# Optimization experiments

Measured on AMD Instinct MI355X. Metric: run time of the kernel, lower is better.

## Reference

```python
import jax, jax.numpy as jnp
import numpy as np

D_MODEL = 1024
N_HEADS = 16
HEAD_DIM = D_MODEL // N_HEADS
NEG = -10000.0  # module uses -10000, not -inf


def setup_inputs() -> dict:
    key = jax.random.key(0)
    ks = jax.random.split(key, 8)
    B, T = 4, 2048
    q = jax.random.normal(ks[0], (B, T, D_MODEL), dtype=jnp.float32)
    k = jax.random.normal(ks[1], (B, T, D_MODEL), dtype=jnp.float32)
    v = jax.random.normal(ks[2], (B, T, D_MODEL), dtype=jnp.float32)
    attn_mask = jnp.ones((B, T), dtype=jnp.float32)
    # xavier_uniform for square [d, d] weights: limit = sqrt(6/(d+d))
    lim = float(np.sqrt(6.0 / (D_MODEL + D_MODEL)))
    Wq = jax.random.uniform(ks[3], (D_MODEL, D_MODEL), jnp.float32, -lim, lim)
    Wk = jax.random.uniform(ks[4], (D_MODEL, D_MODEL), jnp.float32, -lim, lim)
    Wv = jax.random.uniform(ks[5], (D_MODEL, D_MODEL), jnp.float32, -lim, lim)
    Wo = jax.random.uniform(ks[6], (D_MODEL, D_MODEL), jnp.float32, -lim, lim)
    return {"q": q, "k": k, "v": v, "attn_mask": attn_mask,
            "Wq": Wq, "Wk": Wk, "Wv": Wv, "Wo": Wo, "mask_future": 1}


def _split_heads(x):
    B, T, _ = x.shape
    return x.reshape(B, T, N_HEADS, HEAD_DIM).transpose(0, 2, 1, 3)  # [B,H,T,D]


def reference(q, k, v, attn_mask, Wq, Wk, Wv, Wo, mask_future):
    # torch Linear: y = x @ W.T  (weights stored [out, in])
    qh = _split_heads(jnp.einsum('btd,ed->bte', q, Wq))
    kh = _split_heads(jnp.einsum('btd,ed->bte', k, Wk))
    vh = _split_heads(jnp.einsum('btd,ed->bte', v, Wv))
    L, S = qh.shape[-2], kh.shape[-2]
    # dual scale: each of q and k scaled by 1/d**0.25
    scale = 1.0 / jnp.sqrt(jnp.sqrt(jnp.float32(HEAD_DIM)))
    scores = jnp.einsum('bhld,bhsd->bhls', qh * scale, kh * scale)
    if mask_future:
        causal_bias = jnp.triu(jnp.full((L, S), NEG, dtype=scores.dtype), k=1)
        scores = scores + causal_bias
    # padding mask: attn_mask [B, S] -> broadcast [B,1,1,S]; 0 entries -> -10000
    pad = attn_mask[:, None, None, :]
    scores = jnp.where(pad == 0, jnp.asarray(NEG, scores.dtype), scores)
    probs = jax.nn.softmax(scores, axis=-1)  # dropout p=0.0 -> identity
    ctx = jnp.einsum('bhls,bhsd->bhld', probs, vh)
    B = ctx.shape[0]
    ctx = ctx.transpose(0, 2, 1, 3).reshape(B, L, D_MODEL)
    return jnp.einsum('btd,ed->bte', ctx, Wo)
```

## Files before the change

### kernel.cpp

```cpp
#include <hip/hip_runtime.h>

typedef unsigned short u16;
typedef __attribute__((ext_vector_type(8))) _Float16 f16x8;
typedef __attribute__((ext_vector_type(2))) __fp16 fp16v2;
typedef __attribute__((ext_vector_type(4))) float f32x4;

#define T_SEQ 2048
#define NH 16
#define DH 64
#define DM 1024
#define NEG2 (-14426.95f)
#define QS2 (0.42466089f)

__device__ __forceinline__ unsigned pk2(float a, float b) {
  union { fp16v2 v; unsigned u; } c;
  c.v = __builtin_amdgcn_cvt_pkrtz(a, b);
  return c.u;
}
__device__ __forceinline__ u16 f2h(float a) {
  union { _Float16 h; u16 u; } c; c.h = (_Float16)a; return c.u;
}

__device__ __forceinline__ void async_load16(const void* g, void* l) {
  __builtin_amdgcn_global_load_lds(
      (const __attribute__((address_space(1))) unsigned int*)(g),
      (__attribute__((address_space(3))) unsigned int*)(l), 16, 0, 0);
}

__global__ __launch_bounds__(256) void convert_all(
    const float* __restrict__ q, const float* __restrict__ k, const float* __restrict__ v,
    const float* __restrict__ Wq, const float* __restrict__ Wk, const float* __restrict__ Wv,
    const float* __restrict__ Wo, u16* __restrict__ xb, u16* __restrict__ wb) {
  int blk = blockIdx.x;
  const float* src; u16* dst;
  if (blk < 12288) {
    int s = blk >> 12;
    src = (s == 0) ? q : (s == 1) ? k : v;
    dst = xb + (size_t)s * 8388608u;
    blk &= 4095;
  } else {
    int s = (blk - 12288) >> 9;
    src = (s == 0) ? Wq : (s == 1) ? Wk : (s == 2) ? Wv : Wo;
    dst = wb + (size_t)s * 1048576u;
    blk = (blk - 12288) & 511;
  }
  size_t base = (size_t)blk * 2048 + (size_t)threadIdx.x * 8;
  float4 a = *(const float4*)(src + base);
  float4 b2 = *(const float4*)(src + base + 4);
  uint4 st;
  st.x = pk2(a.x, a.y); st.y = pk2(a.z, a.w);
  st.z = pk2(b2.x, b2.y); st.w = pk2(b2.z, b2.w);
  *(uint4*)(dst + base) = st;
}

__global__ __launch_bounds__(256) void gemm_qkv(const u16* __restrict__ A,
                                                const u16* __restrict__ Wqb,
                                                const u16* __restrict__ Wkb,
                                                const u16* __restrict__ Wvb,
                                                u16* __restrict__ Qh, u16* __restrict__ Kh,
                                                u16* __restrict__ VTh) {
  __shared__ char lds[33792];
  const int tid = threadIdx.x;
  const int wid = tid >> 6, lane = tid & 63;
  const int lm = lane & 15, lq = lane >> 4;
  const int m0 = blockIdx.x * 128;
  const int n0 = blockIdx.y * 128;
  const int which = n0 >> 10;
  const int n0l = n0 & 1023;
  const u16* As = A + (size_t)which * 8388608u;
  const u16* Bw = (which == 0) ? Wqb : (which == 1) ? Wkb : Wvb;
  const int wm = wid >> 1, wn = wid & 1;
  char* const rbase = (which < 2) ? (lds + 16384) : lds;
  char* const cbase = (which < 2) ? lds : (lds + 16384);
  f32x4 acc[4][4] = {};

  for (int kt = 0; kt < 1024; kt += 64) {
    __syncthreads();
    for (int i = 0; i < 4; ++i) {
      int p = wid * 4 + i;
      int mt = p >> 1, kk = p & 1;
      int col = kt + kk * 32 + lq * 8;
      async_load16(As + (size_t)(m0 + mt * 16 + lm) * 1024 + col, lds + p * 1024);
      async_load16(Bw + (size_t)(n0l + mt * 16 + lm) * 1024 + col, lds + 16384 + p * 1024);
    }
    __syncthreads();
    for (int kk = 0; kk < 2; ++kk) {
      f16x8 rf[4], cf[4];
      for (int i = 0; i < 4; ++i) {
        rf[i] = *(const f16x8*)(rbase + ((wm * 4 + i) * 2 + kk) * 1024 + lane * 16);
        cf[i] = *(const f16x8*)(cbase + ((wn * 4 + i) * 2 + kk) * 1024 + lane * 16);
      }
      for (int i = 0; i < 4; ++i)
        for (int j = 0; j < 4; ++j)
          acc[i][j] = __builtin_amdgcn_mfma_f32_16x16x32_f16(rf[i], cf[j], acc[i][j], 0, 0, 0);
    }
  }

  const float s = (which < 2) ? QS2 : 1.0f;
  __syncthreads();
  for (int i = 0; i < 4; ++i)
    for (int j = 0; j < 4; ++j) {
      uint2 pv;
      pv.x = pk2(acc[i][j][0] * s, acc[i][j][1] * s);
      pv.y = pk2(acc[i][j][2] * s, acc[i][j][3] * s);
      *(uint2*)(lds + (wn * 64 + j * 16 + lm) * 264 + (wm * 64 + i * 16 + lq * 4) * 2) = pv;
    }
  __syncthreads();

  const int b = m0 >> 11, t0 = m0 & 2047, h0 = n0l >> 6;
  if (which < 2) {
    u16* O = which ? Kh : Qh;
    for (int p = 0; p < 8; ++p) {
      int row = p * 16 + (tid >> 4);
      int seg = tid & 15;
      uint4 val = *(const uint4*)(lds + row * 264 + seg * 16);
      int hl = seg >> 3, dh0 = (seg & 7) * 8;
      *(uint4*)(O + (((size_t)(b * NH + h0 + hl) * T_SEQ + t0 + row) << 6) + dh0) = val;
    }
  } else {
    for (int p = 0; p < 8; ++p) {
      int row = p * 16 + (tid >> 4);
      int seg = tid & 15;
      uint4 val = *(const uint4*)(lds + row * 264 + seg * 16);
      int h = h0 + (row >> 6), dh = row & 63;
      *(uint4*)(VTh + (((size_t)(b * NH + h) * DH + dh) << 11) + t0 + seg * 8) = val;
    }
  }
}

__global__ __launch_bounds__(256) void gemm_out(const u16* __restrict__ A,
                                                const u16* __restrict__ Bw,
                                                float* __restrict__ O) {
  __shared__ char lds[32768];
  const int tid = threadIdx.x;
  const int wid = tid >> 6, lane = tid & 63;
  const int lm = lane & 15, lq = lane >> 4;
  const int m0 = blockIdx.x * 128, n0 = blockIdx.y * 128;
  const int wm = wid >> 1, wn = wid & 1;
  f32x4 acc[4][4] = {};

  for (int kt = 0; kt < 1024; kt += 64) {
    __syncthreads();
    for (int i = 0; i < 4; ++i) {
      int p = wid * 4 + i;
      int mt = p >> 1, kk = p & 1;
      int col = kt + kk * 32 + lq * 8;
      async_load16(A + (size_t)(m0 + mt * 16 + lm) * 1024 + col, lds + p * 1024);
      async_load16(Bw + (size_t)(n0 + mt * 16 + lm) * 1024 + col, lds + 16384 + p * 1024);
    }
    __syncthreads();
    for (int kk = 0; kk < 2; ++kk) {
      f16x8 af[4], bf[4];
      for (int i = 0; i < 4; ++i) {
        af[i] = *(const f16x8*)(lds + ((wm * 4 + i) * 2 + kk) * 1024 + lane * 16);
        bf[i] = *(const f16x8*)(lds + 16384 + ((wn * 4 + i) * 2 + kk) * 1024 + lane * 16);
      }
      for (int i = 0; i < 4; ++i)
        for (int j = 0; j < 4; ++j)
          acc[i][j] = __builtin_amdgcn_mfma_f32_16x16x32_f16(af[i], bf[j], acc[i][j], 0, 0, 0);
    }
  }
  for (int i = 0; i < 4; ++i) {
    int row = m0 + wm * 64 + i * 16 + lq * 4;
    for (int j = 0; j < 4; ++j) {
      int col = n0 + wn * 64 + j * 16 + lm;
      for (int r = 0; r < 4; ++r)
        O[(size_t)(row + r) * 1024 + col] = acc[i][j][r];
    }
  }
}

__global__ __launch_bounds__(256) void attn_kernel(const u16* __restrict__ Qh,
                                                   const u16* __restrict__ Kh,
                                                   const u16* __restrict__ VTh,
                                                   const float* __restrict__ attn_mask,
                                                   const int* __restrict__ mfp,
                                                   u16* __restrict__ ctx) {
  __shared__ char kls[8192];
  __shared__ char vls[8192];
  __shared__ char pls[4][2048];
  __shared__ float maskb[T_SEQ];
  __shared__ int mzf;

  const int tid = threadIdx.x;
  const int wid = tid >> 6, lane = tid & 63;
  const int lm = lane & 15, lq = lane >> 4;
  const int bid = blockIdx.x;
  const int pr = bid & 15, h = (bid >> 4) & 15, b = bid >> 8;
  const int mf = *mfp;
  const size_t bh = (size_t)(b * NH + h);
  const u16* Qbh = Qh + bh * T_SEQ * DH;
  const u16* Kbh = Kh + bh * T_SEQ * DH;
  const u16* VTbh = VTh + bh * DH * T_SEQ;

  if (tid == 0) mzf = 0;
  __syncthreads();
  {
    int az = 0;
    for (int i = tid; i < T_SEQ; i += 256) {
      float mv = attn_mask[(size_t)b * T_SEQ + i];
      maskb[i] = (mv == 0.0f) ? NEG2 : 0.0f;
      az |= (mv == 0.0f);
    }
    if (az) mzf = 1;
  }
  __syncthreads();
  const int maskzero = mzf;

  for (int half = 0; half < 2; ++half) {
    const int qt = half ? (31 - pr) : pr;
    const int q0 = qt * 64;
    const int qw = q0 + wid * 16;
    f16x8 qf[2];
    qf[0] = *(const f16x8*)(Qbh + (size_t)(qw + lm) * DH + lq * 8);
    qf[1] = *(const f16x8*)(Qbh + (size_t)(qw + lm) * DH + 32 + lq * 8);

    f32x4 acc[4] = {};
    float mprev = -1e30f, lsum = 0.f;

    const int nch = mf ? (qt + 1) : 32;
    for (int c = 0; c < nch; ++c) {
      const int s0 = c * 64;
      __syncthreads();
      async_load16(Kbh + (size_t)(s0 + wid * 16 + lm) * DH + lq * 8, kls + (wid * 2 + 0) * 1024);
      async_load16(Kbh + (size_t)(s0 + wid * 16 + lm) * DH + 32 + lq * 8, kls + (wid * 2 + 1) * 1024);
      async_load16(VTbh + (size_t)(wid * 16 + lm) * T_SEQ + s0 + lq * 8, vls + (wid * 2 + 0) * 1024);
      async_load16(VTbh + (size_t)(wid * 16 + lm) * T_SEQ + s0 + 32 + lq * 8, vls + (wid * 2 + 1) * 1024);
      __syncthreads();

      f32x4 sc[4];
      for (int st = 0; st < 4; ++st) {
        f32x4 z = {0.f, 0.f, 0.f, 0.f};
        sc[st] = z;
        for (int kk = 0; kk < 2; ++kk) {
          f16x8 kf = *(const f16x8*)(kls + ((st * 2 + kk) * 64 + lane) * 16);
          sc[st] = __builtin_amdgcn_mfma_f32_16x16x32_f16(kf, qf[kk], sc[st], 0, 0, 0);
        }
      }
      if (maskzero) {
        for (int st = 0; st < 4; ++st) {
          f32x4 mb = *(const f32x4*)(maskb + s0 + st * 16 + lq * 4);
          for (int r = 0; r < 4; ++r) sc[st][r] += mb[r];
        }
      }
      if (mf && (s0 + 64 > qw)) {
        int qg = qw + lm;
        for (int st = 0; st < 4; ++st)
          for (int r = 0; r < 4; ++r)
            if (s0 + st * 16 + lq * 4 + r > qg) sc[st][r] = NEG2;
      }
      float mx = fmaxf(fmaxf(sc[0][0], sc[0][1]), fmaxf(sc[0][2], sc[0][3]));
      for (int st = 1; st < 4; ++st) {
        float t2 = fmaxf(fmaxf(sc[st][0], sc[st][1]), fmaxf(sc[st][2], sc[st][3]));
        mx = fmaxf(mx, t2);
      }
      mx = fmaxf(mx, __shfl_xor(mx, 16));
      mx = fmaxf(mx, __shfl_xor(mx, 32));
      float mn = mprev;
      if (__ballot(mx > mprev) != 0ull) {
        mn = fmaxf(mprev, mx);
        float alpha = exp2f(mprev - mn);
        for (int r = 0; r < 4; ++r) {
          float ar = __shfl(alpha, lq * 4 + r);
          for (int nt = 0; nt < 4; ++nt) acc[nt][r] *= ar;
        }
        lsum *= alpha;
        mprev = mn;
      }
      float ps = 0.f;
      for (int st = 0; st < 4; ++st)
        for (int r = 0; r < 4; ++r) {
          float p = exp2f(sc[st][r] - mn);
          sc[st][r] = p;
          ps += p;
        }
      ps += __shfl_xor(ps, 16);
      ps += __shfl_xor(ps, 32);
      lsum += ps;
      {
        char* pw = pls[wid];
        for (int st = 0; st < 4; ++st) {
          int kk = st >> 1;
          int lqp = (st & 1) * 2 + (lq >> 1);
          uint2 pv;
          pv.x = pk2(sc[st][0], sc[st][1]);
          pv.y = pk2(sc[st][2], sc[st][3]);
          *(uint2*)(pw + kk * 1024 + (lqp * 16 + lm) * 16 + (lq & 1) * 8) = pv;
        }
      }
      asm volatile("s_waitcnt lgkmcnt(0)" ::: "memory");
      for (int kk = 0; kk < 2; ++kk) {
        f16x8 pf = *(const f16x8*)(pls[wid] + kk * 1024 + lane * 16);
        for (int nt = 0; nt < 4; ++nt) {
          f16x8 vf = *(const f16x8*)(vls + ((nt * 2 + kk) * 64 + lane) * 16);
          acc[nt] = __builtin_amdgcn_mfma_f32_16x16x32_f16(pf, vf, acc[nt], 0, 0, 0);
        }
      }
    }
    float inv = 1.0f / lsum;
    for (int r = 0; r < 4; ++r) {
      float ir = __shfl(inv, lq * 4 + r);
      int t = qw + lq * 4 + r;
      for (int nt = 0; nt < 4; ++nt)
        ctx[((size_t)(b * T_SEQ + t) * DM) + h * DH + nt * 16 + lm] = f2h(acc[nt][r] * ir);
    }
  }
}

extern "C" void kernel_launch(void* const* d_in, const int* in_sizes, int n_in,
                              void* d_out, int out_size, void* d_ws, size_t ws_size,
                              hipStream_t stream) {
  const float* q = (const float*)d_in[0];
  const float* k = (const float*)d_in[1];
  const float* v = (const float*)d_in[2];
  const float* attn_mask = (const float*)d_in[3];
  const float* Wq = (const float*)d_in[4];
  const float* Wk = (const float*)d_in[5];
  const float* Wv = (const float*)d_in[6];
  const float* Wo = (const float*)d_in[7];
  const int* mf = (const int*)d_in[8];

  u16* ws = (u16*)d_ws;
  u16* qb  = ws;
  u16* wqb = ws + 3u * 8388608u;
  u16* wkb = wqb + 1048576u;
  u16* wvb = wkb + 1048576u;
  u16* wob = wvb + 1048576u;
  u16* Qh  = wob + 1048576u;
  u16* Kh  = Qh + 8388608u;
  u16* VTh = Kh + 8388608u;
  u16* ctxb = ws;

  convert_all<<<14336, 256, 0, stream>>>(q, k, v, Wq, Wk, Wv, Wo, qb, wqb);

  dim3 gq(64, 24);
  gemm_qkv<<<gq, 256, 0, stream>>>(qb, wqb, wkb, wvb, Qh, Kh, VTh);

  attn_kernel<<<1024, 256, 0, stream>>>(Qh, Kh, VTh, attn_mask, mf, ctxb);

  dim3 gg(64, 8);
  gemm_out<<<gg, 256, 0, stream>>>(ctxb, wob, (float*)d_out);
}
```

Measured before the change: 380.7 us.

## Use 32x32x16 MFMA in GEMMs and 512-thread 128-row attention blocks

Both projection GEMMs switch from 16x16x32 MFMA tiles to 32x32x16 tiles. The LDS staging layout and the epilogue indexing are rewritten to match the new accumulator layout, which should cut LDS fragment reads per MFMA. The attention kernel moves to 512-thread blocks that each handle 128 query rows per pass, so each K/V chunk loaded into LDS is shared by eight waves instead of four. This reduces K/V traffic but halves the grid to 512 blocks and enlarges per-block LDS, which may lower occupancy or leave CUs idle.

```diff
diff --git a/kernel.cpp b/kernel.cpp
--- a/kernel.cpp
+++ b/kernel.cpp
@@ -4,6 +4,7 @@
 typedef __attribute__((ext_vector_type(8))) _Float16 f16x8;
 typedef __attribute__((ext_vector_type(2))) __fp16 fp16v2;
 typedef __attribute__((ext_vector_type(4))) float f32x4;
+typedef __attribute__((ext_vector_type(16))) float f32x16;
 
 #define T_SEQ 2048
 #define NH 16
@@ -62,7 +63,7 @@
   __shared__ char lds[33792];
   const int tid = threadIdx.x;
   const int wid = tid >> 6, lane = tid & 63;
-  const int lm = lane & 15, lq = lane >> 4;
+  const int l32 = lane & 31, lh = lane >> 5;
   const int m0 = blockIdx.x * 128;
   const int n0 = blockIdx.y * 128;
   const int which = n0 >> 10;
@@ -72,38 +73,42 @@
   const int wm = wid >> 1, wn = wid & 1;
   char* const rbase = (which < 2) ? (lds + 16384) : lds;
   char* const cbase = (which < 2) ? lds : (lds + 16384);
-  f32x4 acc[4][4] = {};
+  f32x16 acc[2][2] = {};
 
   for (int kt = 0; kt < 1024; kt += 64) {
     __syncthreads();
     for (int i = 0; i < 4; ++i) {
       int p = wid * 4 + i;
-      int mt = p >> 1, kk = p & 1;
-      int col = kt + kk * 32 + lq * 8;
-      async_load16(As + (size_t)(m0 + mt * 16 + lm) * 1024 + col, lds + p * 1024);
-      async_load16(Bw + (size_t)(n0l + mt * 16 + lm) * 1024 + col, lds + 16384 + p * 1024);
+      int mt = p >> 2, ks = p & 3;
+      int col = kt + ks * 16 + lh * 8;
+      async_load16(As + (size_t)(m0 + mt * 32 + l32) * 1024 + col, lds + p * 1024);
+      async_load16(Bw + (size_t)(n0l + mt * 32 + l32) * 1024 + col, lds + 16384 + p * 1024);
     }
     __syncthreads();
-    for (int kk = 0; kk < 2; ++kk) {
-      f16x8 rf[4], cf[4];
-      for (int i = 0; i < 4; ++i) {
-        rf[i] = *(const f16x8*)(rbase + ((wm * 4 + i) * 2 + kk) * 1024 + lane * 16);
-        cf[i] = *(const f16x8*)(cbase + ((wn * 4 + i) * 2 + kk) * 1024 + lane * 16);
-      }
-      for (int i = 0; i < 4; ++i)
-        for (int j = 0; j < 4; ++j)
-          acc[i][j] = __builtin_amdgcn_mfma_f32_16x16x32_f16(rf[i], cf[j], acc[i][j], 0, 0, 0);
+    for (int ks = 0; ks < 4; ++ks) {
+      f16x8 rf[2], cf[2];
+      for (int i = 0; i < 2; ++i) {
+        rf[i] = *(const f16x8*)(rbase + ((wm * 2 + i) * 4 + ks) * 1024 + lane * 16);
+        cf[i] = *(const f16x8*)(cbase + ((wn * 2 + i) * 4 + ks) * 1024 + lane * 16);
+      }
+      for (int i = 0; i < 2; ++i)
+        for (int j = 0; j < 2; ++j)
+          acc[i][j] = __builtin_amdgcn_mfma_f32_32x32x16_f16(rf[i], cf[j], acc[i][j], 0, 0, 0);
     }
   }
 
   const float s = (which < 2) ? QS2 : 1.0f;
   __syncthreads();
-  for (int i = 0; i < 4; ++i)
-    for (int j = 0; j < 4; ++j) {
-      uint2 pv;
-      pv.x = pk2(acc[i][j][0] * s, acc[i][j][1] * s);
-      pv.y = pk2(acc[i][j][2] * s, acc[i][j][3] * s);
-      *(uint2*)(lds + (wn * 64 + j * 16 + lm) * 264 + (wm * 64 + i * 16 + lq * 4) * 2) = pv;
+  for (int i = 0; i < 2; ++i)
+    for (int j = 0; j < 2; ++j) {
+      int colb = wn * 64 + j * 32 + l32;
+      int rowb = wm * 64 + i * 32 + 4 * lh;
+      for (int g = 0; g < 4; ++g) {
+        uint2 pv;
+        pv.x = pk2(acc[i][j][4 * g + 0] * s, acc[i][j][4 * g + 1] * s);
+        pv.y = pk2(acc[i][j][4 * g + 2] * s, acc[i][j][4 * g + 3] * s);
+        *(uint2*)(lds + colb * 264 + (rowb + 8 * g) * 2) = pv;
+      }
     }
   __syncthreads();
 
@@ -134,43 +139,43 @@
   __shared__ char lds[32768];
   const int tid = threadIdx.x;
   const int wid = tid >> 6, lane = tid & 63;
-  const int lm = lane & 15, lq = lane >> 4;
+  const int l32 = lane & 31, lh = lane >> 5;
   const int m0 = blockIdx.x * 128, n0 = blockIdx.y * 128;
   const int wm = wid >> 1, wn = wid & 1;
-  f32x4 acc[4][4] = {};
+  f32x16 acc[2][2] = {};
 
   for (int kt = 0; kt < 1024; kt += 64) {
     __syncthreads();
     for (int i = 0; i < 4; ++i) {
       int p = wid * 4 + i;
-      int mt = p >> 1, kk = p & 1;
-      int col = kt + kk * 32 + lq * 8;
-      async_load16(A + (size_t)(m0 + mt * 16 + lm) * 1024 + col, lds + p * 1024);
-      async_load16(Bw + (size_t)(n0 + mt * 16 + lm) * 1024 + col, lds + 16384 + p * 1024);
+      int mt = p >> 2, ks = p & 3;
+      int col = kt + ks * 16 + lh * 8;
+      async_load16(A + (size_t)(m0 + mt * 32 + l32) * 1024 + col, lds + p * 1024);
+      async_load16(Bw + (size_t)(n0 + mt * 32 + l32) * 1024 + col, lds + 16384 + p * 1024);
     }
     __syncthreads();
-    for (int kk = 0; kk < 2; ++kk) {
-      f16x8 af[4], bf[4];
-      for (int i = 0; i < 4; ++i) {
-        af[i] = *(const f16x8*)(lds + ((wm * 4 + i) * 2 + kk) * 1024 + lane * 16);
-        bf[i] = *(const f16x8*)(lds + 16384 + ((wn * 4 + i) * 2 + kk) * 1024 + lane * 16);
-      }
-      for (int i = 0; i < 4; ++i)
-        for (int j = 0; j < 4; ++j)
-          acc[i][j] = __builtin_amdgcn_mfma_f32_16x16x32_f16(af[i], bf[j], acc[i][j], 0, 0, 0);
-    }
-  }
-  for (int i = 0; i < 4; ++i) {
-    int row = m0 + wm * 64 + i * 16 + lq * 4;
-    for (int j = 0; j < 4; ++j) {
-      int col = n0 + wn * 64 + j * 16 + lm;
-      for (int r = 0; r < 4; ++r)
-        O[(size_t)(row + r) * 1024 + col] = acc[i][j][r];
-    }
-  }
-}
-
-__global__ __launch_bounds__(256) void attn_kernel(const u16* __restrict__ Qh,
+    for (int ks = 0; ks < 4; ++ks) {
+      f16x8 af[2], bf[2];
+      for (int i = 0; i < 2; ++i) {
+        af[i] = *(const f16x8*)(lds + ((wm * 2 + i) * 4 + ks) * 1024 + lane * 16);
+        bf[i] = *(const f16x8*)(lds + 16384 + ((wn * 2 + i) * 4 + ks) * 1024 + lane * 16);
+      }
+      for (int i = 0; i < 2; ++i)
+        for (int j = 0; j < 2; ++j)
+          acc[i][j] = __builtin_amdgcn_mfma_f32_32x32x16_f16(af[i], bf[j], acc[i][j], 0, 0, 0);
+    }
+  }
+  for (int i = 0; i < 2; ++i)
+    for (int j = 0; j < 2; ++j) {
+      int col = n0 + wn * 64 + j * 32 + l32;
+      int rowb = m0 + wm * 64 + i * 32 + 4 * lh;
+      for (int g = 0; g < 4; ++g)
+        for (int rr = 0; rr < 4; ++rr)
+          O[(size_t)(rowb + 8 * g + rr) * 1024 + col] = acc[i][j][4 * g + rr];
+    }
+}
+
+__global__ __launch_bounds__(512) void attn_kernel(const u16* __restrict__ Qh,
                                                    const u16* __restrict__ Kh,
                                                    const u16* __restrict__ VTh,
                                                    const float* __restrict__ attn_mask,
@@ -178,7 +183,7 @@
                                                    u16* __restrict__ ctx) {
   __shared__ char kls[8192];
   __shared__ char vls[8192];
-  __shared__ char pls[4][2048];
+  __shared__ char pls[8][2048];
   __shared__ float maskb[T_SEQ];
   __shared__ int mzf;
 
@@ -186,7 +191,8 @@
   const int wid = tid >> 6, lane = tid & 63;
   const int lm = lane & 15, lq = lane >> 4;
   const int bid = blockIdx.x;
-  const int pr = bid & 15, h = (bid >> 4) & 15, b = bid >> 8;
+  const int bh_i = bid & 63, p8 = bid >> 6;
+  const int b = bh_i >> 4, h = bh_i & 15;
   const int mf = *mfp;
   const size_t bh = (size_t)(b * NH + h);
   const u16* Qbh = Qh + bh * T_SEQ * DH;
@@ -197,7 +203,7 @@
   __syncthreads();
   {
     int az = 0;
-    for (int i = tid; i < T_SEQ; i += 256) {
+    for (int i = tid; i < T_SEQ; i += 512) {
       float mv = attn_mask[(size_t)b * T_SEQ + i];
       maskb[i] = (mv == 0.0f) ? NEG2 : 0.0f;
       az |= (mv == 0.0f);
@@ -208,8 +214,8 @@
   const int maskzero = mzf;
 
   for (int half = 0; half < 2; ++half) {
-    const int qt = half ? (31 - pr) : pr;
-    const int q0 = qt * 64;
+    const int qt = half ? (15 - p8) : p8;
+    const int q0 = qt * 128;
     const int qw = q0 + wid * 16;
     f16x8 qf[2];
     qf[0] = *(const f16x8*)(Qbh + (size_t)(qw + lm) * DH + lq * 8);
@@ -218,14 +224,14 @@
     f32x4 acc[4] = {};
     float mprev = -1e30f, lsum = 0.f;
 
-    const int nch = mf ? (qt + 1) : 32;
+    const int nch = mf ? (qt + 1) * 2 : 32;
     for (int c = 0; c < nch; ++c) {
       const int s0 = c * 64;
       __syncthreads();
-      async_load16(Kbh + (size_t)(s0 + wid * 16 + lm) * DH + lq * 8, kls + (wid * 2 + 0) * 1024);
-      async_load16(Kbh + (size_t)(s0 + wid * 16 + lm) * DH + 32 + lq * 8, kls + (wid * 2 + 1) * 1024);
-      async_load16(VTbh + (size_t)(wid * 16 + lm) * T_SEQ + s0 + lq * 8, vls + (wid * 2 + 0) * 1024);
-      async_load16(VTbh + (size_t)(wid * 16 + lm) * T_SEQ + s0 + 32 + lq * 8, vls + (wid * 2 + 1) * 1024);
+      async_load16(Kbh + (size_t)(s0 + (wid >> 1) * 16 + lm) * DH + (wid & 1) * 32 + lq * 8,
+                   kls + wid * 1024);
+      async_load16(VTbh + (size_t)((wid >> 1) * 16 + lm) * T_SEQ + s0 + (wid & 1) * 32 + lq * 8,
+                   vls + wid * 1024);
       __syncthreads();
 
       f32x4 sc[4];
@@ -336,7 +342,7 @@
   dim3 gq(64, 24);
   gemm_qkv<<<gq, 256, 0, stream>>>(qb, wqb, wkb, wvb, Qh, Kh, VTh);
 
-  attn_kernel<<<1024, 256, 0, stream>>>(Qh, Kh, VTh, attn_mask, mf, ctxb);
+  attn_kernel<<<512, 512, 0, stream>>>(Qh, Kh, VTh, attn_mask, mf, ctxb);
 
   dim3 gg(64, 8);
   gemm_out<<<gg, 256, 0, stream>>>(ctxb, wob, (float*)d_out);
```

Result: no change. 382.3 us (+0.4%).
